# Kernel optimization log

Measured on AMD Instinct MI355X. Metric: run time of the kernel, lower is better.

Reference implementation:

```python
import jax, jax.numpy as jnp
import numpy as np

TOKEN_DIM = 256
TPR_DIM = 12
INNER_DIM = 256
HID = 32
BN_EPS = 1e-5
SCALE = TOKEN_DIM ** (-0.5)


def setup_inputs() -> dict:
    key = jax.random.key(0)
    ks = jax.random.split(key, 12)
    B, T = 2, 512
    x = jax.random.normal(ks[0], (B, T, TOKEN_DIM), dtype=jnp.float32)
    r = jax.random.normal(ks[1], (B, T, T, TPR_DIM), dtype=jnp.float32)
    # tpr_mlp params
    w1 = jax.random.normal(ks[2], (TPR_DIM, HID), dtype=jnp.float32) * (TPR_DIM ** -0.5)
    b1 = jnp.zeros((HID,), jnp.float32)
    g1 = jnp.ones((HID,), jnp.float32) + 0.1 * jax.random.normal(ks[3], (HID,), dtype=jnp.float32)
    be1 = 0.1 * jax.random.normal(ks[4], (HID,), dtype=jnp.float32)
    m1 = 0.1 * jax.random.normal(ks[5], (HID,), dtype=jnp.float32)
    v1 = jnp.ones((HID,), jnp.float32) + 0.1 * jax.random.uniform(ks[6], (HID,), dtype=jnp.float32)
    w2 = jax.random.normal(ks[7], (HID, TOKEN_DIM), dtype=jnp.float32) * (HID ** -0.5)
    b2 = jnp.zeros((TOKEN_DIM,), jnp.float32)
    g2 = jnp.ones((TOKEN_DIM,), jnp.float32) + 0.1 * jax.random.normal(ks[8], (TOKEN_DIM,), dtype=jnp.float32)
    be2 = 0.1 * jax.random.normal(ks[9], (TOKEN_DIM,), dtype=jnp.float32)
    m2 = 0.1 * jax.random.normal(ks[10], (TOKEN_DIM,), dtype=jnp.float32)
    v2 = jnp.ones((TOKEN_DIM,), jnp.float32) + 0.1 * jax.random.uniform(ks[11], (TOKEN_DIM,), dtype=jnp.float32)
    w_qkv = jax.random.normal(jax.random.fold_in(key, 99), (TOKEN_DIM, 3 * INNER_DIM), dtype=jnp.float32) * (TOKEN_DIM ** -0.5)
    return {"x": x, "r": r, "w1": w1, "b1": b1, "g1": g1, "be1": be1, "m1": m1, "v1": v1,
            "w2": w2, "b2": b2, "g2": g2, "be2": be2, "m2": m2, "v2": v2, "w_qkv": w_qkv}


def _bn_relu(h, g, be, m, v):
    # BatchNorm1d (eval mode, running stats) followed by ReLU; broadcasts over leading dims
    return jax.nn.relu((h - m) * jax.lax.rsqrt(v + BN_EPS) * g + be)


def reference(x, r, w1, b1, g1, be1, m1, v1, w2, b2, g2, be2, m2, v2, w_qkv):
    # TPR MLP over [B,T,T,tpr_dim]
    h = _bn_relu(jnp.einsum('bstd,dh->bsth', r, w1) + b1, g1, be1, m1, v1)   # [B,T,T,HID]
    h = _bn_relu(jnp.einsum('bsth,hc->bstc', h, w2) + b2, g2, be2, m2, v2)    # [B,T,T,C]
    bias = jnp.max(h, axis=2)                                                 # [B,T,C]
    xb = x + bias
    qkv = jnp.einsum('btc,ce->bte', xb, w_qkv)                                # [B,T,3*INNER]
    q, k, v_ = jnp.split(qkv, 3, axis=-1)
    dots = jnp.einsum('btd,bsd->bts', q, k) * SCALE                           # [B,T,T]
    attn = jax.nn.softmax(dots, axis=-1)
    out = jnp.einsum('bts,bsd->btd', attn, v_)                                # [B,T,INNER]
    return out
```

## Files before the change

kernel.cpp:

```cpp
#include <hip/hip_runtime.h>
#include <hip/hip_bf16.h>

#define T 512
#define C 256
#define D12 12
#define HID 32
#define BN_EPS 1e-5f
#define SCALE 0.0625f

typedef __attribute__((ext_vector_type(8))) short bf16x8;
typedef __attribute__((ext_vector_type(4))) float f32x4;

static __device__ __forceinline__ short f2bf(float f) {
    __hip_bfloat16 h = __float2bfloat16(f);
    return *reinterpret_cast<short*>(&h);
}

__global__ __launch_bounds__(256) void k1m_mlp_bias(
    const float* __restrict__ x, const float* __restrict__ r,
    const float* __restrict__ w1, const float* __restrict__ b1,
    const float* __restrict__ g1, const float* __restrict__ be1,
    const float* __restrict__ m1, const float* __restrict__ v1,
    const float* __restrict__ w2, const float* __restrict__ b2,
    const float* __restrict__ g2, const float* __restrict__ be2,
    const float* __restrict__ m2, const float* __restrict__ v2,
    const float* __restrict__ wqkv,
    short* __restrict__ xbb, short* __restrict__ wT)
{
    __shared__ float s1sh[HID];
    __shared__ float C1sh[HID];
    __shared__ short w1t[32 * 32];
    __shared__ short rshbf[64 * 40];
    __shared__ short h1sh[64 * 40];
    __shared__ float biassh[C];
    __shared__ short tsh[64 * 66];

    const int tid  = threadIdx.x;
    const int blk  = blockIdx.x;

    if (blk >= 1024) {
        const int bid2 = blk - 1024;
        const int d0 = (bid2 / 12) * 64;
        const int e0 = (bid2 % 12) * 64;
        #pragma unroll
        for (int i = 0; i < 16; ++i) {
            int idx = i * 256 + tid;
            int di = idx >> 6, ej = idx & 63;
            tsh[di * 66 + ej] = f2bf(wqkv[(size_t)(d0 + di) * 768 + e0 + ej]);
        }
        __syncthreads();
        #pragma unroll
        for (int i = 0; i < 16; ++i) {
            int idx = i * 256 + tid;
            int ei = idx >> 6, dj = idx & 63;
            wT[(size_t)(e0 + ei) * 256 + d0 + dj] = tsh[dj * 66 + ei];
        }
        return;
    }

    const int lane = tid & 63;
    const int wave = tid >> 6;
    const int quad = lane >> 4;
    const int mrow = lane & 15;

    if (tid < HID) {
        float s1 = g1[tid] * rsqrtf(v1[tid] + BN_EPS);
        s1sh[tid] = s1;
        C1sh[tid] = (b1[tid] - m1[tid]) * s1 + be1[tid];
    }
    __syncthreads();

    #pragma unroll
    for (int i = 0; i < 4; ++i) {
        int idx = i * 256 + tid;
        int h = idx >> 5, d = idx & 31;
        float v = (d < D12) ? w1[d * HID + h] * s1sh[h] : 0.f;
        w1t[h * 32 + d] = f2bf(v);
    }
    #pragma unroll
    for (int i = 0; i < 7; ++i) {
        int idx = i * 256 + tid;
        int row = idx / 28, d = 12 + idx % 28;
        rshbf[row * 40 + d] = 0;
    }

    bf16x8 bfrag[4];
    float  c2r[4];
    #pragma unroll
    for (int ct = 0; ct < 4; ++ct) {
        int c = wave * 64 + ct * 16 + mrow;
        float s2 = g2[c] * rsqrtf(v2[c] + BN_EPS);
        c2r[ct] = (b2[c] - m2[c]) * s2 + be2[c];
        #pragma unroll
        for (int j = 0; j < 8; ++j) {
            int k = quad * 8 + j;
            bfrag[ct][j] = f2bf(w2[k * C + c] * s2);
        }
    }
    __syncthreads();

    bf16x8 b1f[2];
    float  c1r[2];
    #pragma unroll
    for (int nt = 0; nt < 2; ++nt) {
        b1f[nt] = *reinterpret_cast<const bf16x8*>(&w1t[(nt * 16 + mrow) * 32 + quad * 8]);
        c1r[nt] = C1sh[nt * 16 + mrow];
    }

    const float* rbase = r + (size_t)blk * T * D12;
    float maxv[4] = {0.f, 0.f, 0.f, 0.f};

    for (int t0 = 0; t0 < T; t0 += 64) {
        #pragma unroll
        for (int i = 0; i < 3; ++i) {
            int idx = i * 256 + tid;
            int row = idx / 12, d = idx - row * 12;
            rshbf[row * 40 + d] = f2bf(rbase[t0 * D12 + idx]);
        }
        __syncthreads();
        {
            bf16x8 af = *reinterpret_cast<const bf16x8*>(
                &rshbf[(wave * 16 + mrow) * 40 + quad * 8]);
            #pragma unroll
            for (int nt = 0; nt < 2; ++nt) {
                f32x4 a = {c1r[nt], c1r[nt], c1r[nt], c1r[nt]};
                a = __builtin_amdgcn_mfma_f32_16x16x32_bf16(af, b1f[nt], a, 0, 0, 0);
                #pragma unroll
                for (int rg = 0; rg < 4; ++rg)
                    h1sh[(wave * 16 + quad * 4 + rg) * 40 + nt * 16 + mrow] =
                        f2bf(fmaxf(a[rg], 0.f));
            }
        }
        __syncthreads();
        #pragma unroll
        for (int rt = 0; rt < 4; ++rt) {
            bf16x8 a2 = *reinterpret_cast<const bf16x8*>(
                &h1sh[(rt * 16 + mrow) * 40 + quad * 8]);
            #pragma unroll
            for (int ct = 0; ct < 4; ++ct) {
                f32x4 acc = {c2r[ct], c2r[ct], c2r[ct], c2r[ct]};
                acc = __builtin_amdgcn_mfma_f32_16x16x32_bf16(a2, bfrag[ct], acc, 0, 0, 0);
                #pragma unroll
                for (int rg = 0; rg < 4; ++rg)
                    maxv[ct] = fmaxf(maxv[ct], acc[rg]);
            }
        }
        __syncthreads();
    }

    #pragma unroll
    for (int ct = 0; ct < 4; ++ct) {
        float m = maxv[ct];
        m = fmaxf(m, __shfl_xor(m, 16));
        m = fmaxf(m, __shfl_xor(m, 32));
        if (quad == 0) biassh[wave * 64 + ct * 16 + mrow] = m;
    }
    __syncthreads();
    xbb[(size_t)blk * C + tid] = f2bf(x[(size_t)blk * C + tid] + biassh[tid]);
}

__global__ __launch_bounds__(256) void k2m_qkv(
    const short* __restrict__ xbb, const short* __restrict__ wT,
    short* __restrict__ qbf, short* __restrict__ vT)
{
    __shared__ short tsh[64 * 66];
    const int tid  = threadIdx.x;
    const int lane = tid & 63;
    const int wave = tid >> 6;
    const int quad = lane >> 4;
    const int mrow = lane & 15;
    const int rb = blockIdx.x / 12;
    const int cb = blockIdx.x % 12;
    const int row0 = rb * 64 + wave * 16;
    const int col0 = cb * 64;
    const float osc = (cb < 4) ? SCALE : 1.0f;

    f32x4 acc[4];
    #pragma unroll
    for (int ct = 0; ct < 4; ++ct) acc[ct] = (f32x4){0.f, 0.f, 0.f, 0.f};

    for (int ks = 0; ks < 8; ++ks) {
        bf16x8 afrag = *reinterpret_cast<const bf16x8*>(
            &xbb[(size_t)(row0 + mrow) * 256 + ks * 32 + quad * 8]);
        #pragma unroll
        for (int ct = 0; ct < 4; ++ct) {
            bf16x8 bfrag = *reinterpret_cast<const bf16x8*>(
                &wT[(size_t)(col0 + ct * 16 + mrow) * 256 + ks * 32 + quad * 8]);
            acc[ct] = __builtin_amdgcn_mfma_f32_16x16x32_bf16(afrag, bfrag, acc[ct], 0, 0, 0);
        }
    }

    if (cb < 8) {
        #pragma unroll
        for (int ct = 0; ct < 4; ++ct)
            #pragma unroll
            for (int rg = 0; rg < 4; ++rg)
                qbf[(size_t)(row0 + quad * 4 + rg) * 768 + col0 + ct * 16 + mrow] =
                    f2bf(acc[ct][rg] * osc);
    } else {
        #pragma unroll
        for (int ct = 0; ct < 4; ++ct)
            #pragma unroll
            for (int rg = 0; rg < 4; ++rg)
                tsh[(wave * 16 + quad * 4 + rg) * 66 + ct * 16 + mrow] = f2bf(acc[ct][rg]);
        __syncthreads();
        const int b  = rb >> 3;
        const int s0 = (rb & 7) * 64;
        const int dg = (cb - 8) * 64;
        #pragma unroll
        for (int i = 0; i < 16; ++i) {
            int idx = i * 256 + tid;
            int ci = idx >> 6, rj = idx & 63;
            vT[((size_t)(b * 256 + dg + ci)) * 512 + s0 + rj] = tsh[rj * 66 + ci];
        }
    }
}

__global__ __launch_bounds__(256) void k3a_attn(
    const short* __restrict__ qbf, const short* __restrict__ vT,
    float* __restrict__ po, float2* __restrict__ stats)
{
    __shared__ float msh[4][16];
    __shared__ float lsh[4][16];
    __shared__ short psh[16 * 136];
    const int tid  = threadIdx.x;
    const int lane = tid & 63;
    const int wave = tid >> 6;
    const int quad = lane >> 4;
    const int mrow = lane & 15;
    const int qt = blockIdx.x >> 2;
    const int sc = blockIdx.x & 3;
    const int b  = qt >> 5;
    const int row0  = qt * 16;
    const int srow0 = b * 512 + sc * 128;

    bf16x8 qf[8];
    {
        const short* qrow = qbf + (size_t)(row0 + mrow) * 768;
        #pragma unroll
        for (int ks = 0; ks < 8; ++ks)
            qf[ks] = *reinterpret_cast<const bf16x8*>(qrow + ks * 32 + quad * 8);
    }

    f32x4 S[2];
    #pragma unroll
    for (int st = 0; st < 2; ++st) {
        f32x4 acc = {0.f, 0.f, 0.f, 0.f};
        const short* krow = qbf + (size_t)(srow0 + wave * 32 + st * 16 + mrow) * 768 + 256;
        #pragma unroll
        for (int ks = 0; ks < 8; ++ks) {
            bf16x8 kf = *reinterpret_cast<const bf16x8*>(krow + ks * 32 + quad * 8);
            acc = __builtin_amdgcn_mfma_f32_16x16x32_bf16(qf[ks], kf, acc, 0, 0, 0);
        }
        S[st] = acc;
    }

    float mx[4];
    #pragma unroll
    for (int rg = 0; rg < 4; ++rg) mx[rg] = fmaxf(S[0][rg], S[1][rg]);
    #pragma unroll
    for (int off = 1; off < 16; off <<= 1)
        #pragma unroll
        for (int rg = 0; rg < 4; ++rg) mx[rg] = fmaxf(mx[rg], __shfl_xor(mx[rg], off));
    if (mrow == 0)
        #pragma unroll
        for (int rg = 0; rg < 4; ++rg) msh[wave][quad * 4 + rg] = mx[rg];
    __syncthreads();

    float M[4], sm[4];
    #pragma unroll
    for (int rg = 0; rg < 4; ++rg) {
        int m = quad * 4 + rg;
        M[rg] = fmaxf(fmaxf(msh[0][m], msh[1][m]), fmaxf(msh[2][m], msh[3][m]));
    }
    float ex[2][4];
    #pragma unroll
    for (int st = 0; st < 2; ++st)
        #pragma unroll
        for (int rg = 0; rg < 4; ++rg) ex[st][rg] = __expf(S[st][rg] - M[rg]);
    #pragma unroll
    for (int rg = 0; rg < 4; ++rg) sm[rg] = ex[0][rg] + ex[1][rg];
    #pragma unroll
    for (int off = 1; off < 16; off <<= 1)
        #pragma unroll
        for (int rg = 0; rg < 4; ++rg) sm[rg] += __shfl_xor(sm[rg], off);
    if (mrow == 0)
        #pragma unroll
        for (int rg = 0; rg < 4; ++rg) lsh[wave][quad * 4 + rg] = sm[rg];
    #pragma unroll
    for (int st = 0; st < 2; ++st)
        #pragma unroll
        for (int rg = 0; rg < 4; ++rg)
            psh[(quad * 4 + rg) * 136 + wave * 32 + st * 16 + mrow] = f2bf(ex[st][rg]);
    __syncthreads();

    if (wave == 0 && mrow == 0) {
        #pragma unroll
        for (int rg = 0; rg < 4; ++rg) {
            int m = quad * 4 + rg;
            float l = lsh[0][m] + lsh[1][m] + lsh[2][m] + lsh[3][m];
            stats[blockIdx.x * 16 + m] = make_float2(M[rg], l);
        }
    }

    const short* vbase = vT + (size_t)b * 256 * 512;
    f32x4 o[4];
    #pragma unroll
    for (int i = 0; i < 4; ++i) o[i] = (f32x4){0.f, 0.f, 0.f, 0.f};
    #pragma unroll
    for (int ks = 0; ks < 4; ++ks) {
        bf16x8 pf = *reinterpret_cast<const bf16x8*>(&psh[mrow * 136 + ks * 32 + quad * 8]);
        #pragma unroll
        for (int i = 0; i < 4; ++i) {
            int d0 = (wave * 4 + i) * 16;
            bf16x8 vf = *reinterpret_cast<const bf16x8*>(
                vbase + (size_t)(d0 + mrow) * 512 + sc * 128 + ks * 32 + quad * 8);
            o[i] = __builtin_amdgcn_mfma_f32_16x16x32_bf16(pf, vf, o[i], 0, 0, 0);
        }
    }
    #pragma unroll
    for (int i = 0; i < 4; ++i)
        #pragma unroll
        for (int rg = 0; rg < 4; ++rg)
            po[((size_t)blockIdx.x * 16 + quad * 4 + rg) * 256 + (wave * 4 + i) * 16 + mrow] =
                o[i][rg];
}

__global__ __launch_bounds__(256) void k3b_combine(
    const float* __restrict__ po, const float2* __restrict__ stats,
    float* __restrict__ out)
{
    const int row = blockIdx.x;
    const int qt = row >> 4, m = row & 15;
    const int c = threadIdx.x;
    float2 s0 = stats[(qt * 4 + 0) * 16 + m];
    float2 s1 = stats[(qt * 4 + 1) * 16 + m];
    float2 s2 = stats[(qt * 4 + 2) * 16 + m];
    float2 s3 = stats[(qt * 4 + 3) * 16 + m];
    float M = fmaxf(fmaxf(s0.x, s1.x), fmaxf(s2.x, s3.x));
    float a0 = __expf(s0.x - M), a1 = __expf(s1.x - M);
    float a2 = __expf(s2.x - M), a3 = __expf(s3.x - M);
    float inv = 1.f / (a0 * s0.y + a1 * s1.y + a2 * s2.y + a3 * s3.y);
    float acc = a0 * po[((size_t)(qt * 4 + 0) * 16 + m) * 256 + c]
              + a1 * po[((size_t)(qt * 4 + 1) * 16 + m) * 256 + c]
              + a2 * po[((size_t)(qt * 4 + 2) * 16 + m) * 256 + c]
              + a3 * po[((size_t)(qt * 4 + 3) * 16 + m) * 256 + c];
    out[(size_t)row * 256 + c] = acc * inv;
}

extern "C" void kernel_launch(void* const* d_in, const int* in_sizes, int n_in,
                              void* d_out, int out_size, void* d_ws, size_t ws_size,
                              hipStream_t stream) {
    const float* x    = (const float*)d_in[0];
    const float* r    = (const float*)d_in[1];
    const float* w1   = (const float*)d_in[2];
    const float* b1   = (const float*)d_in[3];
    const float* g1   = (const float*)d_in[4];
    const float* be1  = (const float*)d_in[5];
    const float* m1   = (const float*)d_in[6];
    const float* v1   = (const float*)d_in[7];
    const float* w2   = (const float*)d_in[8];
    const float* b2   = (const float*)d_in[9];
    const float* g2   = (const float*)d_in[10];
    const float* be2  = (const float*)d_in[11];
    const float* m2   = (const float*)d_in[12];
    const float* v2   = (const float*)d_in[13];
    const float* wqkv = (const float*)d_in[14];
    float* out = (float*)d_out;

    char* ws = (char*)d_ws;
    short*  qbf   = (short*)(ws);
    short*  vT    = (short*)(ws + 1572864);
    short*  xbb   = (short*)(ws + 2097152);
    short*  wT    = (short*)(ws + 2621440);
    float*  po    = (float*)(ws + 3014656);
    float2* stats = (float2*)(ws + 7208960);

    k1m_mlp_bias<<<1072, 256, 0, stream>>>(x, r, w1, b1, g1, be1, m1, v1,
                                           w2, b2, g2, be2, m2, v2, wqkv, xbb, wT);
    k2m_qkv<<<192, 256, 0, stream>>>(xbb, wT, qbf, vT);
    k3a_attn<<<256, 256, 0, stream>>>(qbf, vT, po, stats);
    k3b_combine<<<1024, 256, 0, stream>>>(po, stats, out);
}
```

Measured before the change: 131.0 us.

## Load MLP inputs directly into MFMA fragments and fuse split-K combine into attention

In the MLP kernel, the shared-memory staging of r and of the folded first-layer weights is removed. Each lane now loads its r row straight from global into registers, builds the A fragment there, and prefetches the next tile, which also drops one barrier per iteration. The separate combine kernel is folded into the attention kernel through an atomic counter per query tile: the last of the four split blocks to finish merges the partial outputs and writes the final rows. This saves one kernel launch and the extra pass over the partials, at the cost of a threadfence plus atomic and a serial tail done in a single block per tile.

```diff
diff --git a/kernel.cpp b/kernel.cpp
--- a/kernel.cpp
+++ b/kernel.cpp
@@ -27,10 +27,6 @@
     const float* __restrict__ wqkv,
     short* __restrict__ xbb, short* __restrict__ wT)
 {
-    __shared__ float s1sh[HID];
-    __shared__ float C1sh[HID];
-    __shared__ short w1t[32 * 32];
-    __shared__ short rshbf[64 * 40];
     __shared__ short h1sh[64 * 40];
     __shared__ float biassh[C];
     __shared__ short tsh[64 * 66];
@@ -63,25 +59,18 @@
     const int quad = lane >> 4;
     const int mrow = lane & 15;
 
-    if (tid < HID) {
-        float s1 = g1[tid] * rsqrtf(v1[tid] + BN_EPS);
-        s1sh[tid] = s1;
-        C1sh[tid] = (b1[tid] - m1[tid]) * s1 + be1[tid];
-    }
-    __syncthreads();
-
-    #pragma unroll
-    for (int i = 0; i < 4; ++i) {
-        int idx = i * 256 + tid;
-        int h = idx >> 5, d = idx & 31;
-        float v = (d < D12) ? w1[d * HID + h] * s1sh[h] : 0.f;
-        w1t[h * 32 + d] = f2bf(v);
-    }
-    #pragma unroll
-    for (int i = 0; i < 7; ++i) {
-        int idx = i * 256 + tid;
-        int row = idx / 28, d = 12 + idx % 28;
-        rshbf[row * 40 + d] = 0;
+    bf16x8 b1f[2];
+    float  c1r[2];
+    #pragma unroll
+    for (int nt = 0; nt < 2; ++nt) {
+        int h = nt * 16 + mrow;
+        float s1 = g1[h] * rsqrtf(v1[h] + BN_EPS);
+        c1r[nt] = (b1[h] - m1[h]) * s1 + be1[h];
+        #pragma unroll
+        for (int j = 0; j < 8; ++j) {
+            int k = quad * 8 + j;
+            b1f[nt][j] = (k < D12) ? f2bf(w1[k * HID + h] * s1) : (short)0;
+        }
     }
 
     bf16x8 bfrag[4];
@@ -97,38 +86,49 @@
             bfrag[ct][j] = f2bf(w2[k * C + c] * s2);
         }
     }
-    __syncthreads();
-
-    bf16x8 b1f[2];
-    float  c1r[2];
-    #pragma unroll
-    for (int nt = 0; nt < 2; ++nt) {
-        b1f[nt] = *reinterpret_cast<const bf16x8*>(&w1t[(nt * 16 + mrow) * 32 + quad * 8]);
-        c1r[nt] = C1sh[nt * 16 + mrow];
-    }
 
     const float* rbase = r + (size_t)blk * T * D12;
     float maxv[4] = {0.f, 0.f, 0.f, 0.f};
 
-    for (int t0 = 0; t0 < T; t0 += 64) {
-        #pragma unroll
-        for (int i = 0; i < 3; ++i) {
-            int idx = i * 256 + tid;
-            int row = idx / 12, d = idx - row * 12;
-            rshbf[row * 40 + d] = f2bf(rbase[t0 * D12 + idx]);
-        }
-        __syncthreads();
-        {
-            bf16x8 af = *reinterpret_cast<const bf16x8*>(
-                &rshbf[(wave * 16 + mrow) * 40 + quad * 8]);
+    float v[8];
+    #pragma unroll
+    for (int j = 0; j < 8; ++j) v[j] = 0.f;
+    {
+        const float* rrow = rbase + (size_t)(wave * 16 + mrow) * D12;
+        if (quad == 0) {
+            float4 p0 = *reinterpret_cast<const float4*>(rrow);
+            float4 p1 = *reinterpret_cast<const float4*>(rrow + 4);
+            v[0] = p0.x; v[1] = p0.y; v[2] = p0.z; v[3] = p0.w;
+            v[4] = p1.x; v[5] = p1.y; v[6] = p1.z; v[7] = p1.w;
+        } else if (quad == 1) {
+            float4 p2 = *reinterpret_cast<const float4*>(rrow + 8);
+            v[0] = p2.x; v[1] = p2.y; v[2] = p2.z; v[3] = p2.w;
+        }
+    }
+
+    for (int it = 0; it < 8; ++it) {
+        bf16x8 af;
+        #pragma unroll
+        for (int j = 0; j < 8; ++j) af[j] = f2bf(v[j]);
+        #pragma unroll
+        for (int nt = 0; nt < 2; ++nt) {
+            f32x4 a = {c1r[nt], c1r[nt], c1r[nt], c1r[nt]};
+            a = __builtin_amdgcn_mfma_f32_16x16x32_bf16(af, b1f[nt], a, 0, 0, 0);
             #pragma unroll
-            for (int nt = 0; nt < 2; ++nt) {
-                f32x4 a = {c1r[nt], c1r[nt], c1r[nt], c1r[nt]};
-                a = __builtin_amdgcn_mfma_f32_16x16x32_bf16(af, b1f[nt], a, 0, 0, 0);
-                #pragma unroll
-                for (int rg = 0; rg < 4; ++rg)
-                    h1sh[(wave * 16 + quad * 4 + rg) * 40 + nt * 16 + mrow] =
-                        f2bf(fmaxf(a[rg], 0.f));
+            for (int rg = 0; rg < 4; ++rg)
+                h1sh[(wave * 16 + quad * 4 + rg) * 40 + nt * 16 + mrow] =
+                    f2bf(fmaxf(a[rg], 0.f));
+        }
+        if (it < 7) {
+            const float* rrow = rbase + (size_t)((it + 1) * 64 + wave * 16 + mrow) * D12;
+            if (quad == 0) {
+                float4 p0 = *reinterpret_cast<const float4*>(rrow);
+                float4 p1 = *reinterpret_cast<const float4*>(rrow + 4);
+                v[0] = p0.x; v[1] = p0.y; v[2] = p0.z; v[3] = p0.w;
+                v[4] = p1.x; v[5] = p1.y; v[6] = p1.z; v[7] = p1.w;
+            } else if (quad == 1) {
+                float4 p2 = *reinterpret_cast<const float4*>(rrow + 8);
+                v[0] = p2.x; v[1] = p2.y; v[2] = p2.z; v[3] = p2.w;
             }
         }
         __syncthreads();
@@ -161,7 +161,7 @@
 
 __global__ __launch_bounds__(256) void k2m_qkv(
     const short* __restrict__ xbb, const short* __restrict__ wT,
-    short* __restrict__ qbf, short* __restrict__ vT)
+    short* __restrict__ qbf, short* __restrict__ vT, int* __restrict__ cnt)
 {
     __shared__ short tsh[64 * 66];
     const int tid  = threadIdx.x;
@@ -175,6 +175,8 @@
     const int col0 = cb * 64;
     const float osc = (cb < 4) ? SCALE : 1.0f;
 
+    if (blockIdx.x == 0 && tid < 64) cnt[tid] = 0;
+
     f32x4 acc[4];
     #pragma unroll
     for (int ct = 0; ct < 4; ++ct) acc[ct] = (f32x4){0.f, 0.f, 0.f, 0.f};
@@ -216,13 +218,15 @@
     }
 }
 
-__global__ __launch_bounds__(256) void k3a_attn(
+__global__ __launch_bounds__(256) void k3c_attn(
     const short* __restrict__ qbf, const short* __restrict__ vT,
-    float* __restrict__ po, float2* __restrict__ stats)
+    float* __restrict__ po, float2* __restrict__ stats,
+    int* __restrict__ cnt, float* __restrict__ out)
 {
     __shared__ float msh[4][16];
     __shared__ float lsh[4][16];
     __shared__ short psh[16 * 136];
+    __shared__ int lastsh;
     const int tid  = threadIdx.x;
     const int lane = tid & 63;
     const int wave = tid >> 6;
@@ -324,28 +328,29 @@
         for (int rg = 0; rg < 4; ++rg)
             po[((size_t)blockIdx.x * 16 + quad * 4 + rg) * 256 + (wave * 4 + i) * 16 + mrow] =
                 o[i][rg];
-}
-
-__global__ __launch_bounds__(256) void k3b_combine(
-    const float* __restrict__ po, const float2* __restrict__ stats,
-    float* __restrict__ out)
-{
-    const int row = blockIdx.x;
-    const int qt = row >> 4, m = row & 15;
-    const int c = threadIdx.x;
-    float2 s0 = stats[(qt * 4 + 0) * 16 + m];
-    float2 s1 = stats[(qt * 4 + 1) * 16 + m];
-    float2 s2 = stats[(qt * 4 + 2) * 16 + m];
-    float2 s3 = stats[(qt * 4 + 3) * 16 + m];
-    float M = fmaxf(fmaxf(s0.x, s1.x), fmaxf(s2.x, s3.x));
-    float a0 = __expf(s0.x - M), a1 = __expf(s1.x - M);
-    float a2 = __expf(s2.x - M), a3 = __expf(s3.x - M);
-    float inv = 1.f / (a0 * s0.y + a1 * s1.y + a2 * s2.y + a3 * s3.y);
-    float acc = a0 * po[((size_t)(qt * 4 + 0) * 16 + m) * 256 + c]
-              + a1 * po[((size_t)(qt * 4 + 1) * 16 + m) * 256 + c]
-              + a2 * po[((size_t)(qt * 4 + 2) * 16 + m) * 256 + c]
-              + a3 * po[((size_t)(qt * 4 + 3) * 16 + m) * 256 + c];
-    out[(size_t)row * 256 + c] = acc * inv;
+
+    __threadfence();
+    __syncthreads();
+    if (tid == 0) lastsh = (atomicAdd(&cnt[qt], 1) == 3);
+    __syncthreads();
+    if (!lastsh) return;
+    __threadfence();
+
+    for (int m = 0; m < 16; ++m) {
+        float2 s0 = stats[(qt * 4 + 0) * 16 + m];
+        float2 s1 = stats[(qt * 4 + 1) * 16 + m];
+        float2 s2 = stats[(qt * 4 + 2) * 16 + m];
+        float2 s3 = stats[(qt * 4 + 3) * 16 + m];
+        float Mm = fmaxf(fmaxf(s0.x, s1.x), fmaxf(s2.x, s3.x));
+        float a0 = __expf(s0.x - Mm), a1 = __expf(s1.x - Mm);
+        float a2 = __expf(s2.x - Mm), a3 = __expf(s3.x - Mm);
+        float inv = 1.f / (a0 * s0.y + a1 * s1.y + a2 * s2.y + a3 * s3.y);
+        float accv = a0 * po[((size_t)(qt * 4 + 0) * 16 + m) * 256 + tid]
+                   + a1 * po[((size_t)(qt * 4 + 1) * 16 + m) * 256 + tid]
+                   + a2 * po[((size_t)(qt * 4 + 2) * 16 + m) * 256 + tid]
+                   + a3 * po[((size_t)(qt * 4 + 3) * 16 + m) * 256 + tid];
+        out[(size_t)(row0 + m) * 256 + tid] = accv * inv;
+    }
 }
 
 extern "C" void kernel_launch(void* const* d_in, const int* in_sizes, int n_in,
@@ -375,10 +380,10 @@
     short*  wT    = (short*)(ws + 2621440);
     float*  po    = (float*)(ws + 3014656);
     float2* stats = (float2*)(ws + 7208960);
+    int*    cnt   = (int*)(ws + 7241728);
 
     k1m_mlp_bias<<<1072, 256, 0, stream>>>(x, r, w1, b1, g1, be1, m1, v1,
                                            w2, b2, g2, be2, m2, v2, wqkv, xbb, wT);
-    k2m_qkv<<<192, 256, 0, stream>>>(xbb, wT, qbf, vT);
-    k3a_attn<<<256, 256, 0, stream>>>(qbf, vT, po, stats);
-    k3b_combine<<<1024, 256, 0, stream>>>(po, stats, out);
-}
+    k2m_qkv<<<192, 256, 0, stream>>>(xbb, wT, qbf, vT, cnt);
+    k3c_attn<<<256, 256, 0, stream>>>(qbf, vT, po, stats, cnt, out);
+}
```

Measured after the change: 175.7 us. +34.2%, slower.
